# Kernel optimization log

Hardware: AMD Instinct MI355X
Metric: run time of the kernel (lower is better)

## Reference

```python
import jax, jax.numpy as jnp
import numpy as np

B, L, D, V, C = 16384, 50, 128, 91718, 11
H, HD, F = 4, 32, 6
NP = F * (F - 1) // 2  # 15 pairs
CIN = F * D + NP * D   # 2688


def setup_inputs() -> dict:
    key = jax.random.key(0)
    ks = jax.random.split(key, 32)
    inp = {}
    inp['item_id'] = jax.random.randint(ks[0], (B,), 0, V)
    inp['item_mm'] = jax.random.normal(ks[1], (B, D), dtype=jnp.float32)
    inp['likes'] = jax.random.randint(ks[2], (B,), 0, C)
    inp['views'] = jax.random.randint(ks[3], (B,), 0, C)
    inp['item_seq'] = jax.random.randint(ks[4], (B, L), 0, V)
    g = lambda k, shape, s: (jax.random.normal(k, shape, dtype=jnp.float32) * s)
    inp['item_emb'] = g(ks[5], (V, D), 0.02).at[0].set(0.0)  # padding_idx=0
    inp['cate_emb'] = g(ks[6], (C, D), 0.02)
    inp['mm_w'] = g(ks[7], (D, D), (2.0 / D) ** 0.5)
    inp['mm_b'] = jnp.zeros((D,), jnp.float32)
    inp['ln_g'] = jnp.ones((D,), jnp.float32)
    inp['ln_b'] = jnp.zeros((D,), jnp.float32)
    inp['gnn_W'] = g(ks[8], (H, D, HD), (2.0 / (D + HD)) ** 0.5 * 1.414)
    inp['gnn_a'] = g(ks[9], (H, 2 * HD, 1), 0.1)
    inp['se_w1'] = g(ks[10], (F, F // 2), 0.4)
    inp['se_b1'] = jnp.zeros((F // 2,), jnp.float32)
    inp['se_w2'] = g(ks[11], (F // 2, F), 0.4)
    inp['se_b2'] = jnp.zeros((F,), jnp.float32)
    inp['bi_W'] = g(ks[12], (F - 1, D, D), (2.0 / (2 * D)) ** 0.5)
    inp['mlp_w1'] = g(ks[13], (CIN, 512), (2.0 / CIN) ** 0.5)
    inp['mlp_b1'] = jnp.zeros((512,), jnp.float32)
    inp['bn1_g'] = jnp.ones((512,), jnp.float32)
    inp['bn1_b'] = jnp.zeros((512,), jnp.float32)
    inp['mlp_w2'] = g(ks[14], (512, 256), (2.0 / 512) ** 0.5)
    inp['mlp_b2'] = jnp.zeros((256,), jnp.float32)
    inp['bn2_g'] = jnp.ones((256,), jnp.float32)
    inp['bn2_b'] = jnp.zeros((256,), jnp.float32)
    inp['mlp_w3'] = g(ks[15], (256, 1), (2.0 / 256) ** 0.5)
    inp['mlp_b3'] = jnp.zeros((1,), jnp.float32)
    return inp


def _forward(item_id, item_mm, likes, views, item_seq,
             item_emb, cate_emb, mm_w, mm_b, ln_g, ln_b,
             gnn_W, gnn_a, se_w1, se_b1, se_w2, se_b2, bi_W,
             mlp_w1, mlp_b1, bn1_g, bn1_b, mlp_w2, mlp_b2, bn2_g, bn2_b,
             mlp_w3, mlp_b3):
    bsz = item_id.shape[0]
    eps = 1e-5

    user_feat = jnp.zeros((bsz, D), item_mm.dtype)
    like_feat = cate_emb[likes]
    view_feat = cate_emb[views]
    id_feat = item_emb[item_id]

    # mm_proj: Linear -> LayerNorm -> GELU (exact)
    y = item_mm @ mm_w + mm_b
    mu = y.mean(-1, keepdims=True)
    var = y.var(-1, keepdims=True)
    y = (y - mu) * jax.lax.rsqrt(var + eps) * ln_g + ln_b
    img_feat = jax.nn.gelu(y, approximate=False)

    # masked mean pooling of history
    seq_emb = item_emb[item_seq]                          # [B,L,D]
    mask = item_seq == 0
    seq_emb = jnp.where(mask[..., None], 0.0, seq_emb)
    cnt = jnp.clip(jnp.sum((~mask).astype(seq_emb.dtype), axis=1, keepdims=True), 1.0)
    hist_feat = seq_emb.sum(1) / cnt

    x = jnp.stack([user_feat, like_feat, view_feat, id_feat, img_feat, hist_feat], axis=1)  # [B,6,D]

    # GAT over 6-node fully-connected feature graph
    hp = jnp.einsum('bni,hio->bnho', x, gnn_W)            # [B,6,H,HD]
    a1 = gnn_a[:, :HD, 0]                                  # [H,HD]
    a2 = gnn_a[:, HD:, 0]
    ei = jnp.einsum('bnhd,hd->bhn', hp, a1)
    ej = jnp.einsum('bnhd,hd->bhn', hp, a2)
    e = ei[:, :, :, None] + ej[:, :, None, :]             # [B,H,6,6]
    e = jnp.where(e > 0, e, 0.2 * e)                       # LeakyReLU(0.2)
    att = jax.nn.softmax(e, axis=-1)                       # dropout off (eval)
    h_new = jnp.einsum('bhnm,bmho->bnho', att, hp).reshape(bsz, F, D)
    gnn_feat = jax.nn.elu(h_new + x)                       # in_dim == out_dim

    # SENet
    z = gnn_feat.mean(-1)                                  # [B,6]
    w = jax.nn.sigmoid(jax.nn.relu(z @ se_w1 + se_b1) @ se_w2 + se_b2)
    s = gnn_feat * w[..., None]

    # Bilinear ('each'): vid_i = s_i @ W_i, pairs (i,j), j>i
    vid = jnp.einsum('bfd,fde->bfe', s[:, :F - 1], bi_W)   # [B,5,D]
    p = jnp.stack([vid[:, i] * s[:, j] for i in range(F - 1) for j in range(i + 1, F)], axis=1)  # [B,15,D]

    c = jnp.concatenate([gnn_feat.reshape(bsz, -1), p.reshape(bsz, -1)], axis=1)  # [B,2688]

    # MLP with eval-mode BatchNorm (running mean 0, var 1) and dropout off
    bn = lambda t, g_, b_: t * (g_ / jnp.sqrt(1.0 + eps)) + b_
    h1 = jax.nn.gelu(bn(c @ mlp_w1 + mlp_b1, bn1_g, bn1_b), approximate=False)
    h2 = jax.nn.gelu(bn(h1 @ mlp_w2 + mlp_b2, bn2_g, bn2_b), approximate=False)
    out = jax.nn.sigmoid(h2 @ mlp_w3 + mlp_b3)
    return out.squeeze(-1)


def reference(item_id, item_mm, likes, views, item_seq,
              item_emb, cate_emb, mm_w, mm_b, ln_g, ln_b,
              gnn_W, gnn_a, se_w1, se_b1, se_w2, se_b2, bi_W,
              mlp_w1, mlp_b1, bn1_g, bn1_b, mlp_w2, mlp_b2, bn2_g, bn2_b,
              mlp_w3, mlp_b3):
    return _forward(item_id, item_mm, likes, views, item_seq,
                    item_emb, cate_emb, mm_w, mm_b, ln_g, ln_b,
                    gnn_W, gnn_a, se_w1, se_b1, se_w2, se_b2, bi_W,
                    mlp_w1, mlp_b1, bn1_g, bn1_b, mlp_w2, mlp_b2, bn2_g, bn2_b,
                    mlp_w3, mlp_b3)
```

## Files before the change

kernel.cpp:

```cpp
#include <hip/hip_runtime.h>
#include <hip/hip_bf16.h>
#include <cstdint>
#include <cstddef>

#define BB 16384

typedef float  floatx4 __attribute__((ext_vector_type(4)));
typedef __bf16 bf16x8  __attribute__((ext_vector_type(8)));

__device__ __forceinline__ unsigned short f2bf(float f) {
  union { float f; unsigned int u; } v; v.f = f;
  unsigned int r = v.u + 0x7FFFu + ((v.u >> 16) & 1u);
  return (unsigned short)(r >> 16);
}
__device__ __forceinline__ float bf2f(unsigned short h) {
  union { unsigned int u; float f; } v; v.u = ((unsigned int)h) << 16;
  return v.f;
}
__device__ __forceinline__ float gelu_exact(float x) {
  return 0.5f * x * (1.0f + erff(x * 0.7071067811865475f));
}

#define ALOAD16(g, l) \
  __builtin_amdgcn_global_load_lds((const __attribute__((address_space(1))) void*)(g), \
                                   (__attribute__((address_space(3))) void*)(l), 16, 0, 0)

__global__ void k_pack(const float* __restrict__ mm_w, const float* __restrict__ gnn_W,
                       const float* __restrict__ bi_W, const float* __restrict__ item_mm,
                       const float* __restrict__ item_emb,
                       unsigned short* __restrict__ mmwt, unsigned short* __restrict__ wallt,
                       unsigned short* __restrict__ biwt, unsigned short* __restrict__ immb,
                       unsigned short* __restrict__ iembb)
{
  const int total = 2211840 + 2934976;
  for (int id = blockIdx.x * 256 + threadIdx.x; id < total; id += gridDim.x * 256) {
    if (id < 16384) {
      int n = id / 128, k = id % 128;
      mmwt[id] = f2bf(mm_w[k * 128 + n]);
    } else if (id < 32768) {
      int l = id - 16384; int nc = l / 128, k = l % 128;
      wallt[l] = f2bf(gnn_W[(nc >> 5) * 4096 + k * 32 + (nc & 31)]);
    } else if (id < 114688) {
      int l = id - 32768; int f = l / 16384, rr = l % 16384, e = rr / 128, d = rr % 128;
      biwt[l] = f2bf(bi_W[f * 16384 + d * 128 + e]);
    } else if (id < 2211840) {
      int l = id - 114688;
      immb[l] = f2bf(item_mm[l]);
    } else {
      int l = id - 2211840;
      float4 v = ((const float4*)item_emb)[l];
      ushort4 o; o.x = f2bf(v.x); o.y = f2bf(v.y); o.z = f2bf(v.z); o.w = f2bf(v.w);
      ((ushort4*)iembb)[l] = o;
    }
  }
}

__global__ __launch_bounds__(256)
void k_transp2(const float* __restrict__ w1, const float* __restrict__ w2,
               unsigned short* __restrict__ w1t, unsigned short* __restrict__ w2t)
{
  __shared__ float tile[64][65];
  int blk = blockIdx.x;
  const float* in; unsigned short* outp; int R, C, bx, by;
  if (blk < 336) { in = w1; outp = w1t; R = 2688; C = 512; bx = blk % 8; by = blk / 8; }
  else { blk -= 336; in = w2; outp = w2t; R = 512; C = 256; bx = blk % 4; by = blk / 4; }
  const int c0 = bx * 64, r0 = by * 64;
  const int lr = threadIdx.x >> 6;
  const int lc = threadIdx.x & 63;
  #pragma unroll
  for (int i = 0; i < 16; i++) {
    int r = lr + i * 4;
    tile[r][lc] = in[(size_t)(r0 + r) * C + c0 + lc];
  }
  __syncthreads();
  #pragma unroll
  for (int i = 0; i < 16; i++) {
    int c = lr + i * 4;
    outp[(size_t)(c0 + c) * R + r0 + lc] = f2bf(tile[lc][c]);
  }
}

template<int BM, int EPI, bool SWZ>
__global__ __launch_bounds__(512)
void gemm_bt(const unsigned short* __restrict__ A, int lda,
             const unsigned short* __restrict__ Bt, int ldb,
             void* __restrict__ Cp, int ldc, int K,
             const float* __restrict__ bias, const float* __restrict__ bng,
             const float* __restrict__ bnb)
{
  constexpr int WGM = BM / 64;
  constexpr int WGN = 8 / WGM;
  constexpr int TN  = 128 / WGN;
  constexpr int NT  = TN / 16;
  constexpr int NRW = (BM + 128) / 8;
  constexpr int ISS = NRW / 8;

  int bx = blockIdx.x, by = blockIdx.y;
  if constexpr (SWZ) {
    int p = by * gridDim.x + bx;
    int xcd = p & 7, slot = p >> 3;
    bx = slot % gridDim.x;
    by = xcd * (gridDim.y >> 3) + slot / gridDim.x;
  }
  const int n0 = bx * 128;
  const int m0 = by * BM;
  __shared__ __align__(16) unsigned short As[BM * 64];
  __shared__ __align__(16) unsigned short Bs[128 * 64];
  const int t = threadIdx.x;
  const int lane = t & 63, w = t >> 6;
  const int wm = w % WGM, wn = w / WGM;
  const int lr = lane & 15, lq = lane >> 4;

  floatx4 acc[4][NT];
  #pragma unroll
  for (int a = 0; a < 4; a++)
    #pragma unroll
    for (int b = 0; b < NT; b++) acc[a][b] = (floatx4){0.f, 0.f, 0.f, 0.f};

  const int srow = lane >> 3;
  const int schk = (lane & 7) ^ srow;
  const int rb0 = w * NRW;

  for (int k0 = 0; k0 < K; k0 += 64) {
    __syncthreads();
    #pragma unroll
    for (int q = 0; q < ISS; q++) {
      const int rb = rb0 + q * 8;
      if (rb < BM) {
        ALOAD16(A + (size_t)(m0 + rb + srow) * lda + k0 + schk * 8, As + rb * 64);
      } else {
        const int rbb = rb - BM;
        ALOAD16(Bt + (size_t)(n0 + rbb + srow) * ldb + k0 + schk * 8, Bs + rbb * 64);
      }
    }
    __syncthreads();
    #pragma unroll
    for (int ko = 0; ko < 2; ko++) {
      bf16x8 af[4], bfv[NT];
      #pragma unroll
      for (int mt = 0; mt < 4; mt++) {
        const int row = wm * 64 + mt * 16 + lr;
        const int pc = (ko * 4 + lq) ^ (lr & 7);
        af[mt] = __builtin_bit_cast(bf16x8, *(const uint4*)&As[row * 64 + pc * 8]);
      }
      #pragma unroll
      for (int nt = 0; nt < NT; nt++) {
        const int row = wn * TN + nt * 16 + lr;
        const int pc = (ko * 4 + lq) ^ (lr & 7);
        bfv[nt] = __builtin_bit_cast(bf16x8, *(const uint4*)&Bs[row * 64 + pc * 8]);
      }
      #pragma unroll
      for (int mt = 0; mt < 4; mt++)
        #pragma unroll
        for (int nt = 0; nt < NT; nt++)
          acc[mt][nt] = __builtin_amdgcn_mfma_f32_16x16x32_bf16(af[mt], bfv[nt], acc[mt][nt], 0, 0, 0);
    }
  }

  #pragma unroll
  for (int mt = 0; mt < 4; mt++)
    #pragma unroll
    for (int nt = 0; nt < NT; nt++)
      #pragma unroll
      for (int i = 0; i < 4; i++) {
        const int cm = m0 + wm * 64 + mt * 16 + lq * 4 + i;
        const int cn = n0 + wn * TN + nt * 16 + lr;
        float v = acc[mt][nt][i];
        size_t idx = (size_t)cm * ldc + cn;
        float tt = v + bias[cn];
        tt = tt * (bng[cn] * 0.9999950000374997f) + bnb[cn];
        ((unsigned short*)Cp)[idx] = f2bf(gelu_exact(tt));
      }
}

__global__ __launch_bounds__(512)
void k_mmln(const unsigned short* __restrict__ A, const unsigned short* __restrict__ Bt,
            const float* __restrict__ mm_b, const float* __restrict__ ln_g,
            const float* __restrict__ ln_b, unsigned short* __restrict__ xb)
{
  __shared__ __align__(16) char smem[64 * 130 * 4];
  unsigned short* As = (unsigned short*)smem;
  unsigned short* Bs = (unsigned short*)(smem + 8192);
  float* cls = (float*)smem;

  const int t = threadIdx.x, lane = t & 63, w = t >> 6;
  const int lr = lane & 15, lq = lane >> 4;
  const int m0 = blockIdx.x * 64;

  floatx4 acc[4];
  #pragma unroll
  for (int a = 0; a < 4; a++) acc[a] = (floatx4){0.f, 0.f, 0.f, 0.f};

  const int srow = lane >> 3;
  const int schk = (lane & 7) ^ srow;
  const int rb0 = w * 24;

  for (int k0 = 0; k0 < 128; k0 += 64) {
    __syncthreads();
    #pragma unroll
    for (int q = 0; q < 3; q++) {
      const int rb = rb0 + q * 8;
      if (rb < 64) ALOAD16(A + (size_t)(m0 + rb + srow) * 128 + k0 + schk * 8, As + rb * 64);
      else { const int rbb = rb - 64; ALOAD16(Bt + (size_t)(rbb + srow) * 128 + k0 + schk * 8, Bs + rbb * 64); }
    }
    __syncthreads();
    #pragma unroll
    for (int ko = 0; ko < 2; ko++) {
      bf16x8 af[4], bv;
      #pragma unroll
      for (int mt = 0; mt < 4; mt++) {
        const int row = mt * 16 + lr;
        const int pc = (ko * 4 + lq) ^ (lr & 7);
        af[mt] = __builtin_bit_cast(bf16x8, *(const uint4*)&As[row * 64 + pc * 8]);
      }
      {
        const int row = w * 16 + lr;
        const int pc = (ko * 4 + lq) ^ (lr & 7);
        bv = __builtin_bit_cast(bf16x8, *(const uint4*)&Bs[row * 64 + pc * 8]);
      }
      #pragma unroll
      for (int mt = 0; mt < 4; mt++)
        acc[mt] = __builtin_amdgcn_mfma_f32_16x16x32_bf16(af[mt], bv, acc[mt], 0, 0, 0);
    }
  }

  __syncthreads();
  #pragma unroll
  for (int mt = 0; mt < 4; mt++)
    #pragma unroll
    for (int i = 0; i < 4; i++) {
      const int rr = mt * 16 + lq * 4 + i;
      const int cc = w * 16 + lr;
      cls[rr * 130 + cc] = acc[mt][i] + mm_b[cc];
    }
  __syncthreads();

  const float2 g2 = *(const float2*)&ln_g[lane * 2];
  const float2 b2 = *(const float2*)&ln_b[lane * 2];
  #pragma unroll
  for (int rr = 0; rr < 8; rr++) {
    const int r = w * 8 + rr;
    float2 v = *(const float2*)&cls[r * 130 + lane * 2];
    float s = v.x + v.y, s2 = v.x * v.x + v.y * v.y;
    #pragma unroll
    for (int o = 32; o > 0; o >>= 1) { s += __shfl_xor(s, o, 64); s2 += __shfl_xor(s2, o, 64); }
    float mu  = s * (1.0f / 128.0f);
    float var = s2 * (1.0f / 128.0f) - mu * mu;
    float rs  = rsqrtf(var + 1e-5f);
    float t0 = gelu_exact((v.x - mu) * rs * g2.x + b2.x);
    float t1 = gelu_exact((v.y - mu) * rs * g2.y + b2.y);
    unsigned int pk = (unsigned int)f2bf(t0) | ((unsigned int)f2bf(t1) << 16);
    *(unsigned int*)&xb[(size_t)(m0 + r) * 768 + 512 + lane * 2] = pk;
  }
}

__global__ __launch_bounds__(256)
void k_hpatt(const unsigned short* __restrict__ xb, const unsigned short* __restrict__ wallt,
             const float* __restrict__ gnn_a, const float* __restrict__ se_w1,
             const float* __restrict__ se_b1, const float* __restrict__ se_w2,
             const float* __restrict__ se_b2, unsigned short* __restrict__ c,
             unsigned short* __restrict__ sb)
{
  __shared__ __align__(16) char smem[52992];
  unsigned short* As = (unsigned short*)smem;
  unsigned short* Bs = (unsigned short*)(smem + 12288);
  float* hps  = (float*)smem;
  float* eis  = (float*)(smem + 49920);
  float* ejs  = eis + 96;
  float* atts = ejs + 96;

  const int t = threadIdx.x, lane = t & 63, w = t >> 6;
  const int wm = w & 1, wn = w >> 1;
  const int lr = lane & 15, lq = lane >> 4;
  const int m0 = blockIdx.x * 96;

  floatx4 acc[3][4];
  #pragma unroll
  for (int a = 0; a < 3; a++)
    #pragma unroll
    for (int b = 0; b < 4; b++) acc[a][b] = (floatx4){0.f, 0.f, 0.f, 0.f};

  const int srow = lane >> 3;
  const int schk = (lane & 7) ^ srow;
  const int rb0 = w * 56;

  for (int k0 = 0; k0 < 128; k0 += 64) {
    __syncthreads();
    #pragma unroll
    for (int q = 0; q < 7; q++) {
      const int rb = rb0 + q * 8;
      if (rb < 96) ALOAD16(xb + (size_t)(m0 + rb + srow) * 128 + k0 + schk * 8, As + rb * 64);
      else { const int rbb = rb - 96; ALOAD16(wallt + (size_t)(rbb + srow) * 128 + k0 + schk * 8, Bs + rbb * 64); }
    }
    __syncthreads();
    #pragma unroll
    for (int ko = 0; ko < 2; ko++) {
      bf16x8 af[3], bfv[4];
      #pragma unroll
      for (int mt = 0; mt < 3; mt++) {
        const int row = wm * 48 + mt * 16 + lr;
        const int pc = (ko * 4 + lq) ^ (lr & 7);
        af[mt] = __builtin_bit_cast(bf16x8, *(const uint4*)&As[row * 64 + pc * 8]);
      }
      #pragma unroll
      for (int nt = 0; nt < 4; nt++) {
        const int row = wn * 64 + nt * 16 + lr;
        const int pc = (ko * 4 + lq) ^ (lr & 7);
        bfv[nt] = __builtin_bit_cast(bf16x8, *(const uint4*)&Bs[row * 64 + pc * 8]);
      }
      #pragma unroll
      for (int mt = 0; mt < 3; mt++)
        #pragma unroll
        for (int nt = 0; nt < 4; nt++)
          acc[mt][nt] = __builtin_amdgcn_mfma_f32_16x16x32_bf16(af[mt], bfv[nt], acc[mt][nt], 0, 0, 0);
    }
  }

  __syncthreads();
  #pragma unroll
  for (int mt = 0; mt < 3; mt++)
    #pragma unroll
    for (int nt = 0; nt < 4; nt++)
      #pragma unroll
      for (int i = 0; i < 4; i++) {
        const int rr = wm * 48 + mt * 16 + lq * 4 + i;
        const int cc = wn * 64 + nt * 16 + lr;
        hps[rr * 130 + cc] = acc[mt][nt][i];
      }
  __syncthreads();

  for (int it = 0; it < 4; it++) {
    const int lb = w * 4 + it;
    const int b = blockIdx.x * 16 + lb;
    const float* hb = hps + lb * 6 * 130;

    if (lane < 24) {
      int h = lane & 3, n = lane >> 2;
      float e1 = 0.f, e2 = 0.f;
      for (int o = 0; o < 32; o++) {
        float v = hb[n * 130 + h * 32 + o];
        e1 += v * gnn_a[h * 64 + o];
        e2 += v * gnn_a[h * 64 + 32 + o];
      }
      eis[w * 24 + h * 6 + n] = e1; ejs[w * 24 + h * 6 + n] = e2;
    }
    if (lane < 24) {
      int h = lane & 3, i = lane >> 2;
      float ev[6]; float mx = -1e30f;
      #pragma unroll
      for (int j = 0; j < 6; j++) {
        float e = eis[w * 24 + h * 6 + i] + ejs[w * 24 + h * 6 + j];
        e = e > 0.f ? e : 0.2f * e;
        ev[j] = e; mx = fmaxf(mx, e);
      }
      float ssum = 0.f;
      #pragma unroll
      for (int j = 0; j < 6; j++) { ev[j] = expf(ev[j] - mx); ssum += ev[j]; }
      float inv = 1.0f / ssum;
      #pragma unroll
      for (int j = 0; j < 6; j++) atts[w * 144 + h * 36 + i * 6 + j] = ev[j] * inv;
    }

    const int hh = lane >> 4;
    float g0[6], g1[6], zz[6];
    #pragma unroll
    for (int n = 0; n < 6; n++) {
      float hn0 = 0.f, hn1 = 0.f;
      #pragma unroll
      for (int m = 0; m < 6; m++) {
        float a = atts[w * 144 + hh * 36 + n * 6 + m];
        float2 v = *(const float2*)&hb[m * 130 + lane * 2];
        hn0 += a * v.x; hn1 += a * v.y;
      }
      unsigned int xp = *(const unsigned int*)&xb[(size_t)b * 768 + n * 128 + lane * 2];
      float a0 = hn0 + bf2f((unsigned short)(xp & 0xFFFFu));
      float a1 = hn1 + bf2f((unsigned short)(xp >> 16));
      a0 = a0 > 0.f ? a0 : expm1f(a0);
      a1 = a1 > 0.f ? a1 : expm1f(a1);
      g0[n] = a0; g1[n] = a1;
      float zacc = a0 + a1;
      #pragma unroll
      for (int o = 32; o > 0; o >>= 1) zacc += __shfl_xor(zacc, o, 64);
      zz[n] = zacc * (1.0f / 128.0f);
    }

    float rr3[3];
    #pragma unroll
    for (int j = 0; j < 3; j++) {
      float a = se_b1[j];
      #pragma unroll
      for (int n = 0; n < 6; n++) a += zz[n] * se_w1[n * 3 + j];
      rr3[j] = fmaxf(a, 0.f);
    }
    float wse[6];
    #pragma unroll
    for (int n = 0; n < 6; n++) {
      float a = se_b2[n];
      #pragma unroll
      for (int j = 0; j < 3; j++) a += rr3[j] * se_w2[j * 6 + n];
      wse[n] = 1.0f / (1.0f + expf(-a));
    }

    #pragma unroll
    for (int n = 0; n < 6; n++) {
      unsigned int pc = (unsigned int)f2bf(g0[n]) | ((unsigned int)f2bf(g1[n]) << 16);
      unsigned int ps = (unsigned int)f2bf(g0[n] * wse[n]) | ((unsigned int)f2bf(g1[n] * wse[n]) << 16);
      *(unsigned int*)&c[(size_t)b * 2688 + n * 128 + lane * 2]  = pc;
      *(unsigned int*)&sb[(size_t)b * 768 + n * 128 + lane * 2]  = ps;
    }
  }
}

__global__ __launch_bounds__(256)
void gemm_vid(const unsigned short* __restrict__ sbb, const unsigned short* __restrict__ biwt,
              unsigned short* __restrict__ c)
{
  const int z = blockIdx.z;
  const int m0 = blockIdx.y * 128;
  __shared__ __align__(16) unsigned short smem[128 * 130];
  unsigned short* As = smem;
  unsigned short* Bs = smem + 8192;
  const int t = threadIdx.x;
  const int lane = t & 63, w = t >> 6;
  const int wm = w & 1, wn = w >> 1;
  const int lr = lane & 15, lq = lane >> 4;

  floatx4 acc[4][4];
  #pragma unroll
  for (int a = 0; a < 4; a++)
    #pragma unroll
    for (int b = 0; b < 4; b++) acc[a][b] = (floatx4){0.f, 0.f, 0.f, 0.f};

  const int srow = lane >> 3;
  const int schk = (lane & 7) ^ srow;
  const unsigned short* Ag = sbb + (size_t)(m0 + w * 32 + srow) * 768 + z * 128 + schk * 8;
  const unsigned short* Bg = biwt + z * 16384 + (size_t)(w * 32 + srow) * 128 + schk * 8;
  unsigned short* AsW = As + w * 32 * 64;
  unsigned short* BsW = Bs + w * 32 * 64;

  for (int k0 = 0; k0 < 128; k0 += 64) {
    __syncthreads();
    #pragma unroll
    for (int q = 0; q < 4; q++) {
      ALOAD16(Ag + k0 + (size_t)(q * 8) * 768, AsW + q * 512);
      ALOAD16(Bg + k0 + (size_t)(q * 8) * 128, BsW + q * 512);
    }
    __syncthreads();
    #pragma unroll
    for (int ko = 0; ko < 2; ko++) {
      bf16x8 af[4], bfv[4];
      #pragma unroll
      for (int mt = 0; mt < 4; mt++) {
        const int row = wm * 64 + mt * 16 + lr;
        const int pc = (ko * 4 + lq) ^ (lr & 7);
        af[mt] = __builtin_bit_cast(bf16x8, *(const uint4*)&As[row * 64 + pc * 8]);
      }
      #pragma unroll
      for (int nt = 0; nt < 4; nt++) {
        const int row = wn * 64 + nt * 16 + lr;
        const int pc = (ko * 4 + lq) ^ (lr & 7);
        bfv[nt] = __builtin_bit_cast(bf16x8, *(const uint4*)&Bs[row * 64 + pc * 8]);
      }
      #pragma unroll
      for (int mt = 0; mt < 4; mt++)
        #pragma unroll
        for (int nt = 0; nt < 4; nt++)
          acc[mt][nt] = __builtin_amdgcn_mfma_f32_16x16x32_bf16(af[mt], bfv[nt], acc[mt][nt], 0, 0, 0);
    }
  }

  __syncthreads();
  #pragma unroll
  for (int mt = 0; mt < 4; mt++)
    #pragma unroll
    for (int nt = 0; nt < 4; nt++)
      #pragma unroll
      for (int i = 0; i < 4; i++) {
        const int rr = wm * 64 + mt * 16 + lq * 4 + i;
        const int cc = wn * 64 + nt * 16 + lr;
        smem[rr * 130 + cc] = f2bf(acc[mt][nt][i]);
      }
  __syncthreads();

  const int pb0[5] = {0, 5, 9, 12, 14};
  const int npairs = 5 - z;
  const int tot = 128 * 32 * npairs;
  for (int e = t; e < tot; e += 256) {
    const int g  = e & 31;
    const int rp = e >> 5;
    const int p  = rp % npairs;
    const int r  = rp / npairs;
    ushort4 vv = *(const ushort4*)&smem[r * 130 + g * 4];
    ushort4 sv = *(const ushort4*)&sbb[(size_t)(m0 + r) * 768 + (z + 1 + p) * 128 + g * 4];
    ushort4 o;
    o.x = f2bf(bf2f(vv.x) * bf2f(sv.x));
    o.y = f2bf(bf2f(vv.y) * bf2f(sv.y));
    o.z = f2bf(bf2f(vv.z) * bf2f(sv.z));
    o.w = f2bf(bf2f(vv.w) * bf2f(sv.w));
    *(ushort4*)&c[(size_t)(m0 + r) * 2688 + 768 + (size_t)(pb0[z] + p) * 128 + g * 4] = o;
  }
}

__global__ __launch_bounds__(256)
void k_feat(const int* __restrict__ item_id, const int* __restrict__ likes,
            const int* __restrict__ views, const int* __restrict__ item_seq,
            const unsigned short* __restrict__ iembb, const float* __restrict__ cate_emb,
            unsigned short* __restrict__ xb)
{
  const int b = blockIdx.x * 4 + (threadIdx.x >> 6);
  const int lane = threadIdx.x & 63;
  const int half = lane >> 5, ql = lane & 31;
  const size_t base = (size_t)b * 768;
  const int li = likes[b], vi = views[b], id = item_id[b];

  int idxs[25];
  #pragma unroll
  for (int j = 0; j < 25; j++) idxs[j] = item_seq[b * 50 + half + 2 * j];

  float4 hs = make_float4(0.f, 0.f, 0.f, 0.f);
  float cnt = 0.f;
  #pragma unroll
  for (int j = 0; j < 25; j++) {
    const int idx = idxs[j];
    if (idx != 0) {
      cnt += 1.0f;
      ushort4 v = *(const ushort4*)&iembb[(size_t)idx * 128 + ql * 4];
      hs.x += bf2f(v.x); hs.y += bf2f(v.y); hs.z += bf2f(v.z); hs.w += bf2f(v.w);
    }
  }
  cnt  += __shfl_xor(cnt, 32, 64);
  hs.x += __shfl_xor(hs.x, 32, 64);
  hs.y += __shfl_xor(hs.y, 32, 64);
  hs.z += __shfl_xor(hs.z, 32, 64);
  hs.w += __shfl_xor(hs.w, 32, 64);
  const float ic = 1.0f / fmaxf(cnt, 1.0f);

  *(unsigned int*)&xb[base + lane * 2] = 0u;

  {
    const float4 v = *(const float4*)&cate_emb[(size_t)(half ? vi : li) * 128 + ql * 4];
    ushort4 o; o.x = f2bf(v.x); o.y = f2bf(v.y); o.z = f2bf(v.z); o.w = f2bf(v.w);
    *(ushort4*)&xb[base + 128 + half * 128 + ql * 4] = o;
  }
  if (half == 0) {
    *(ushort4*)&xb[base + 384 + ql * 4] =
        *(const ushort4*)&iembb[(size_t)id * 128 + ql * 4];
  } else {
    ushort4 o; o.x = f2bf(hs.x * ic); o.y = f2bf(hs.y * ic);
               o.z = f2bf(hs.z * ic); o.w = f2bf(hs.w * ic);
    *(ushort4*)&xb[base + 640 + ql * 4] = o;
  }
}

__global__ __launch_bounds__(512)
void k_mlp2out(const unsigned short* __restrict__ A, const unsigned short* __restrict__ Bt,
               const float* __restrict__ b2v, const float* __restrict__ bng,
               const float* __restrict__ bnb, const float* __restrict__ w3,
               const float* __restrict__ b3, float* __restrict__ out)
{
  __shared__ __align__(16) char smem[40960];
  unsigned short* As = (unsigned short*)smem;
  unsigned short* Bs = (unsigned short*)(smem + 8192);
  unsigned short* h2s = (unsigned short*)smem;

  const int t = threadIdx.x, lane = t & 63, w = t >> 6;
  const int lr = lane & 15, lq = lane >> 4;
  const int m0 = blockIdx.x * 64;

  floatx4 acc[4][2];
  #pragma unroll
  for (int a = 0; a < 4; a++)
    #pragma unroll
    for (int b = 0; b < 2; b++) acc[a][b] = (floatx4){0.f, 0.f, 0.f, 0.f};

  const int srow = lane >> 3;
  const int schk = (lane & 7) ^ srow;
  const int rb0 = w * 40;

  for (int k0 = 0; k0 < 512; k0 += 64) {
    __syncthreads();
    #pragma unroll
    for (int q = 0; q < 5; q++) {
      const int rb = rb0 + q * 8;
      if (rb < 64) ALOAD16(A + (size_t)(m0 + rb + srow) * 512 + k0 + schk * 8, As + rb * 64);
      else { const int rbb = rb - 64; ALOAD16(Bt + (size_t)(rbb + srow) * 512 + k0 + schk * 8, Bs + rbb * 64); }
    }
    __syncthreads();
    #pragma unroll
    for (int ko = 0; ko < 2; ko++) {
      bf16x8 af[4], bfv[2];
      #pragma unroll
      for (int mt = 0; mt < 4; mt++) {
        const int row = mt * 16 + lr;
        const int pc = (ko * 4 + lq) ^ (lr & 7);
        af[mt] = __builtin_bit_cast(bf16x8, *(const uint4*)&As[row * 64 + pc * 8]);
      }
      #pragma unroll
      for (int nt = 0; nt < 2; nt++) {
        const int row = w * 32 + nt * 16 + lr;
        const int pc = (ko * 4 + lq) ^ (lr & 7);
        bfv[nt] = __builtin_bit_cast(bf16x8, *(const uint4*)&Bs[row * 64 + pc * 8]);
      }
      #pragma unroll
      for (int mt = 0; mt < 4; mt++)
        #pragma unroll
        for (int nt = 0; nt < 2; nt++)
          acc[mt][nt] = __builtin_amdgcn_mfma_f32_16x16x32_bf16(af[mt], bfv[nt], acc[mt][nt], 0, 0, 0);
    }
  }

  __syncthreads();
  #pragma unroll
  for (int mt = 0; mt < 4; mt++)
    #pragma unroll
    for (int nt = 0; nt < 2; nt++)
      #pragma unroll
      for (int i = 0; i < 4; i++) {
        const int rr = mt * 16 + lq * 4 + i;
        const int cc = w * 32 + nt * 16 + lr;
        float tt = acc[mt][nt][i] + b2v[cc];
        tt = tt * (bng[cc] * 0.9999950000374997f) + bnb[cc];
        h2s[rr * 264 + cc] = f2bf(gelu_exact(tt));
      }
  __syncthreads();

  const float4 w4 = *(const float4*)&w3[lane * 4];
  #pragma unroll
  for (int rr = 0; rr < 8; rr++) {
    const int r = w * 8 + rr;
    ushort4 v = *(const ushort4*)&h2s[r * 264 + lane * 4];
    float a = bf2f(v.x) * w4.x + bf2f(v.y) * w4.y + bf2f(v.z) * w4.z + bf2f(v.w) * w4.w;
    #pragma unroll
    for (int o = 32; o > 0; o >>= 1) a += __shfl_xor(a, o, 64);
    if (lane == 0) out[m0 + r] = 1.0f / (1.0f + expf(-(a + b3[0])));
  }
}

#define OFF_MMWT   0ull
#define OFF_WALLT  32768ull
#define OFF_BIWT   65536ull
#define OFF_W1T    229376ull
#define OFF_W2T    2981888ull
#define OFF_IMMB   3244032ull
#define OFF_XB     7438336ull
#define OFF_SB     57769984ull
#define OFF_C      82935808ull
#define OFF_IEMB   179404800ull

extern "C" void kernel_launch(void* const* d_in, const int* in_sizes, int n_in,
                              void* d_out, int out_size, void* d_ws, size_t ws_size,
                              hipStream_t stream)
{
  const int*   item_id  = (const int*)  d_in[0];
  const float* item_mm  = (const float*)d_in[1];
  const int*   likes    = (const int*)  d_in[2];
  const int*   views    = (const int*)  d_in[3];
  const int*   item_seq = (const int*)  d_in[4];
  const float* item_emb = (const float*)d_in[5];
  const float* cate_emb = (const float*)d_in[6];
  const float* mm_w     = (const float*)d_in[7];
  const float* mm_b     = (const float*)d_in[8];
  const float* ln_g     = (const float*)d_in[9];
  const float* ln_b     = (const float*)d_in[10];
  const float* gnn_W    = (const float*)d_in[11];
  const float* gnn_a    = (const float*)d_in[12];
  const float* se_w1    = (const float*)d_in[13];
  const float* se_b1    = (const float*)d_in[14];
  const float* se_w2    = (const float*)d_in[15];
  const float* se_b2    = (const float*)d_in[16];
  const float* bi_W     = (const float*)d_in[17];
  const float* mlp_w1   = (const float*)d_in[18];
  const float* mlp_b1   = (const float*)d_in[19];
  const float* bn1_g    = (const float*)d_in[20];
  const float* bn1_b    = (const float*)d_in[21];
  const float* mlp_w2   = (const float*)d_in[22];
  const float* mlp_b2   = (const float*)d_in[23];
  const float* bn2_g    = (const float*)d_in[24];
  const float* bn2_b    = (const float*)d_in[25];
  const float* mlp_w3   = (const float*)d_in[26];
  const float* mlp_b3   = (const float*)d_in[27];
  float* out = (float*)d_out;

  char* ws = (char*)d_ws;
  unsigned short* mmwt  = (unsigned short*)(ws + OFF_MMWT);
  unsigned short* wallt = (unsigned short*)(ws + OFF_WALLT);
  unsigned short* biwt  = (unsigned short*)(ws + OFF_BIWT);
  unsigned short* w1t   = (unsigned short*)(ws + OFF_W1T);
  unsigned short* w2t   = (unsigned short*)(ws + OFF_W2T);
  unsigned short* immb  = (unsigned short*)(ws + OFF_IMMB);
  unsigned short* xb    = (unsigned short*)(ws + OFF_XB);
  unsigned short* sbb   = (unsigned short*)(ws + OFF_SB);
  unsigned short* cbuf  = (unsigned short*)(ws + OFF_C);
  unsigned short* h1b   = (unsigned short*)(ws + OFF_XB);
  unsigned short* iembb = (unsigned short*)(ws + OFF_IEMB);

  k_pack<<<4096, 256, 0, stream>>>(mm_w, gnn_W, bi_W, item_mm, item_emb,
                                   mmwt, wallt, biwt, immb, iembb);
  k_transp2<<<368, 256, 0, stream>>>(mlp_w1, mlp_w2, w1t, w2t);
  k_feat<<<BB / 4, 256, 0, stream>>>(item_id, likes, views, item_seq, iembb, cate_emb, xb);
  k_mmln<<<256, 512, 0, stream>>>(immb, mmwt, mm_b, ln_g, ln_b, xb);
  k_hpatt<<<1024, 256, 0, stream>>>(xb, wallt, gnn_a, se_w1, se_b1, se_w2, se_b2, cbuf, sbb);
  gemm_vid<<<dim3(1, 128, 5), 256, 0, stream>>>(sbb, biwt, cbuf);
  gemm_bt<128, 3, true><<<dim3(4, 128), 512, 0, stream>>>(cbuf, 2688, w1t, 2688,
      h1b, 512, 2688, mlp_b1, bn1_g, bn1_b);
  k_mlp2out<<<256, 512, 0, stream>>>(h1b, w2t, mlp_b2, bn2_g, bn2_b, mlp_w3, mlp_b3, out);
}
```

Measured before the change: 347.2 us.

## Deepen MLP1 GEMM K-tile to 128 and move small weight transposes into tiled kernel

The MLP1 GEMM is specialised to fixed sizes and loads a K depth of 128 per iteration instead of 64. This halves the number of barrier-separated load/compute rounds, at the cost of doubling LDS use to 64 KB per block, which may reduce occupancy. The bi_W and mm_w transposes move from the strided element-wise pack loop into the shared-memory tiled transpose kernel. The item_mm bf16 conversion is also vectorised to float4 loads.

```diff
diff --git a/kernel.cpp b/kernel.cpp
--- a/kernel.cpp
+++ b/kernel.cpp
@@ -25,29 +25,23 @@
   __builtin_amdgcn_global_load_lds((const __attribute__((address_space(1))) void*)(g), \
                                    (__attribute__((address_space(3))) void*)(l), 16, 0, 0)
 
-__global__ void k_pack(const float* __restrict__ mm_w, const float* __restrict__ gnn_W,
-                       const float* __restrict__ bi_W, const float* __restrict__ item_mm,
+__global__ void k_pack(const float* __restrict__ gnn_W, const float* __restrict__ item_mm,
                        const float* __restrict__ item_emb,
-                       unsigned short* __restrict__ mmwt, unsigned short* __restrict__ wallt,
-                       unsigned short* __restrict__ biwt, unsigned short* __restrict__ immb,
+                       unsigned short* __restrict__ wallt, unsigned short* __restrict__ immb,
                        unsigned short* __restrict__ iembb)
 {
-  const int total = 2211840 + 2934976;
+  const int total = 16384 + 524288 + 2934976;
   for (int id = blockIdx.x * 256 + threadIdx.x; id < total; id += gridDim.x * 256) {
     if (id < 16384) {
-      int n = id / 128, k = id % 128;
-      mmwt[id] = f2bf(mm_w[k * 128 + n]);
-    } else if (id < 32768) {
-      int l = id - 16384; int nc = l / 128, k = l % 128;
-      wallt[l] = f2bf(gnn_W[(nc >> 5) * 4096 + k * 32 + (nc & 31)]);
-    } else if (id < 114688) {
-      int l = id - 32768; int f = l / 16384, rr = l % 16384, e = rr / 128, d = rr % 128;
-      biwt[l] = f2bf(bi_W[f * 16384 + d * 128 + e]);
-    } else if (id < 2211840) {
-      int l = id - 114688;
-      immb[l] = f2bf(item_mm[l]);
+      int nc = id / 128, k = id % 128;
+      wallt[id] = f2bf(gnn_W[(nc >> 5) * 4096 + k * 32 + (nc & 31)]);
+    } else if (id < 540672) {
+      int l = id - 16384;
+      float4 v = ((const float4*)item_mm)[l];
+      ushort4 o; o.x = f2bf(v.x); o.y = f2bf(v.y); o.z = f2bf(v.z); o.w = f2bf(v.w);
+      ((ushort4*)immb)[l] = o;
     } else {
-      int l = id - 2211840;
+      int l = id - 540672;
       float4 v = ((const float4*)item_emb)[l];
       ushort4 o; o.x = f2bf(v.x); o.y = f2bf(v.y); o.z = f2bf(v.z); o.w = f2bf(v.w);
       ((ushort4*)iembb)[l] = o;
@@ -57,13 +51,20 @@
 
 __global__ __launch_bounds__(256)
 void k_transp2(const float* __restrict__ w1, const float* __restrict__ w2,
-               unsigned short* __restrict__ w1t, unsigned short* __restrict__ w2t)
+               const float* __restrict__ bi_W, const float* __restrict__ mm_w,
+               unsigned short* __restrict__ w1t, unsigned short* __restrict__ w2t,
+               unsigned short* __restrict__ biwt, unsigned short* __restrict__ mmwt)
 {
   __shared__ float tile[64][65];
   int blk = blockIdx.x;
   const float* in; unsigned short* outp; int R, C, bx, by;
-  if (blk < 336) { in = w1; outp = w1t; R = 2688; C = 512; bx = blk % 8; by = blk / 8; }
-  else { blk -= 336; in = w2; outp = w2t; R = 512; C = 256; bx = blk % 4; by = blk / 4; }
+  if (blk < 336)      { in = w1; outp = w1t; R = 2688; C = 512; bx = blk % 8; by = blk / 8; }
+  else if (blk < 368) { blk -= 336; in = w2; outp = w2t; R = 512; C = 256; bx = blk % 4; by = blk / 4; }
+  else if (blk < 388) { blk -= 368; int f = blk / 4; int r2 = blk % 4;
+                        in = bi_W + f * 16384; outp = biwt + f * 16384;
+                        R = 128; C = 128; bx = r2 % 2; by = r2 / 2; }
+  else                { blk -= 388; in = mm_w; outp = mmwt; R = 128; C = 128;
+                        bx = blk % 2; by = blk / 2; }
   const int c0 = bx * 64, r0 = by * 64;
   const int lr = threadIdx.x >> 6;
   const int lc = threadIdx.x & 63;
@@ -80,79 +81,67 @@
   }
 }
 
-template<int BM, int EPI, bool SWZ>
 __global__ __launch_bounds__(512)
-void gemm_bt(const unsigned short* __restrict__ A, int lda,
-             const unsigned short* __restrict__ Bt, int ldb,
-             void* __restrict__ Cp, int ldc, int K,
-             const float* __restrict__ bias, const float* __restrict__ bng,
-             const float* __restrict__ bnb)
-{
-  constexpr int WGM = BM / 64;
-  constexpr int WGN = 8 / WGM;
-  constexpr int TN  = 128 / WGN;
-  constexpr int NT  = TN / 16;
-  constexpr int NRW = (BM + 128) / 8;
-  constexpr int ISS = NRW / 8;
-
-  int bx = blockIdx.x, by = blockIdx.y;
-  if constexpr (SWZ) {
-    int p = by * gridDim.x + bx;
-    int xcd = p & 7, slot = p >> 3;
-    bx = slot % gridDim.x;
-    by = xcd * (gridDim.y >> 3) + slot / gridDim.x;
-  }
+void gemm_mlp1(const unsigned short* __restrict__ A, const unsigned short* __restrict__ Bt,
+               unsigned short* __restrict__ Cp,
+               const float* __restrict__ bias, const float* __restrict__ bng,
+               const float* __restrict__ bnb)
+{
+  int p = blockIdx.y * gridDim.x + blockIdx.x;
+  int xcd = p & 7, slot = p >> 3;
+  const int bx = slot % gridDim.x;
+  const int by = xcd * (gridDim.y >> 3) + slot / gridDim.x;
   const int n0 = bx * 128;
-  const int m0 = by * BM;
-  __shared__ __align__(16) unsigned short As[BM * 64];
-  __shared__ __align__(16) unsigned short Bs[128 * 64];
-  const int t = threadIdx.x;
-  const int lane = t & 63, w = t >> 6;
-  const int wm = w % WGM, wn = w / WGM;
+  const int m0 = by * 128;
+
+  __shared__ __align__(16) unsigned short As[128 * 128];
+  __shared__ __align__(16) unsigned short Bs[128 * 128];
+  const int t = threadIdx.x, lane = t & 63, w = t >> 6;
+  const int wm = w & 1, wn = w >> 1;
   const int lr = lane & 15, lq = lane >> 4;
 
-  floatx4 acc[4][NT];
+  floatx4 acc[4][2];
   #pragma unroll
   for (int a = 0; a < 4; a++)
     #pragma unroll
-    for (int b = 0; b < NT; b++) acc[a][b] = (floatx4){0.f, 0.f, 0.f, 0.f};
-
-  const int srow = lane >> 3;
-  const int schk = (lane & 7) ^ srow;
-  const int rb0 = w * NRW;
-
-  for (int k0 = 0; k0 < K; k0 += 64) {
-    __syncthreads();
-    #pragma unroll
-    for (int q = 0; q < ISS; q++) {
-      const int rb = rb0 + q * 8;
-      if (rb < BM) {
-        ALOAD16(A + (size_t)(m0 + rb + srow) * lda + k0 + schk * 8, As + rb * 64);
+    for (int b = 0; b < 2; b++) acc[a][b] = (floatx4){0.f, 0.f, 0.f, 0.f};
+
+  const int srow = lane >> 4;
+  const int rb0 = w * 32;
+
+  for (int k0 = 0; k0 < 2688; k0 += 128) {
+    __syncthreads();
+    #pragma unroll
+    for (int q = 0; q < 8; q++) {
+      const int rb = rb0 + q * 4;
+      const int row = rb + srow;
+      const int schk = (lane & 15) ^ (row & 7);
+      if (rb < 128) {
+        ALOAD16(A + (size_t)(m0 + row) * 2688 + k0 + schk * 8, As + rb * 128);
       } else {
-        const int rbb = rb - BM;
-        ALOAD16(Bt + (size_t)(n0 + rbb + srow) * ldb + k0 + schk * 8, Bs + rbb * 64);
-      }
-    }
-    __syncthreads();
-    #pragma unroll
-    for (int ko = 0; ko < 2; ko++) {
-      bf16x8 af[4], bfv[NT];
+        ALOAD16(Bt + (size_t)(n0 + row - 128) * 2688 + k0 + schk * 8, Bs + (rb - 128) * 128);
+      }
+    }
+    __syncthreads();
+    #pragma unroll
+    for (int ko = 0; ko < 4; ko++) {
+      bf16x8 af[4], bfv[2];
       #pragma unroll
       for (int mt = 0; mt < 4; mt++) {
         const int row = wm * 64 + mt * 16 + lr;
-        const int pc = (ko * 4 + lq) ^ (lr & 7);
-        af[mt] = __builtin_bit_cast(bf16x8, *(const uint4*)&As[row * 64 + pc * 8]);
-      }
-      #pragma unroll
-      for (int nt = 0; nt < NT; nt++) {
-        const int row = wn * TN + nt * 16 + lr;
-        const int pc = (ko * 4 + lq) ^ (lr & 7);
-        bfv[nt] = __builtin_bit_cast(bf16x8, *(const uint4*)&Bs[row * 64 + pc * 8]);
+        const int pc = (ko * 4 + lq) ^ (row & 7);
+        af[mt] = __builtin_bit_cast(bf16x8, *(const uint4*)&As[row * 128 + pc * 8]);
+      }
+      #pragma unroll
+      for (int nt = 0; nt < 2; nt++) {
+        const int row = wn * 32 + nt * 16 + lr;
+        const int pc = (ko * 4 + lq) ^ (row & 7);
+        bfv[nt] = __builtin_bit_cast(bf16x8, *(const uint4*)&Bs[row * 128 + pc * 8]);
       }
       #pragma unroll
       for (int mt = 0; mt < 4; mt++)
         #pragma unroll
-        for (int nt = 0; nt < NT; nt++)
+        for (int nt = 0; nt < 2; nt++)
           acc[mt][nt] = __builtin_amdgcn_mfma_f32_16x16x32_bf16(af[mt], bfv[nt], acc[mt][nt], 0, 0, 0);
     }
   }
@@ -160,16 +149,14 @@
   #pragma unroll
   for (int mt = 0; mt < 4; mt++)
     #pragma unroll
-    for (int nt = 0; nt < NT; nt++)
+    for (int nt = 0; nt < 2; nt++)
       #pragma unroll
       for (int i = 0; i < 4; i++) {
         const int cm = m0 + wm * 64 + mt * 16 + lq * 4 + i;
-        const int cn = n0 + wn * TN + nt * 16 + lr;
-        float v = acc[mt][nt][i];
-        size_t idx = (size_t)cm * ldc + cn;
-        float tt = v + bias[cn];
+        const int cn = n0 + wn * 32 + nt * 16 + lr;
+        float tt = acc[mt][nt][i] + bias[cn];
         tt = tt * (bng[cn] * 0.9999950000374997f) + bnb[cn];
-        ((unsigned short*)Cp)[idx] = f2bf(gelu_exact(tt));
+        Cp[(size_t)cm * 512 + cn] = f2bf(gelu_exact(tt));
       }
 }
 
@@ -694,14 +681,12 @@
   unsigned short* h1b   = (unsigned short*)(ws + OFF_XB);
   unsigned short* iembb = (unsigned short*)(ws + OFF_IEMB);
 
-  k_pack<<<4096, 256, 0, stream>>>(mm_w, gnn_W, bi_W, item_mm, item_emb,
-                                   mmwt, wallt, biwt, immb, iembb);
-  k_transp2<<<368, 256, 0, stream>>>(mlp_w1, mlp_w2, w1t, w2t);
+  k_pack<<<4096, 256, 0, stream>>>(gnn_W, item_mm, item_emb, wallt, immb, iembb);
+  k_transp2<<<392, 256, 0, stream>>>(mlp_w1, mlp_w2, bi_W, mm_w, w1t, w2t, biwt, mmwt);
   k_feat<<<BB / 4, 256, 0, stream>>>(item_id, likes, views, item_seq, iembb, cate_emb, xb);
   k_mmln<<<256, 512, 0, stream>>>(immb, mmwt, mm_b, ln_g, ln_b, xb);
   k_hpatt<<<1024, 256, 0, stream>>>(xb, wallt, gnn_a, se_w1, se_b1, se_w2, se_b2, cbuf, sbb);
   gemm_vid<<<dim3(1, 128, 5), 256, 0, stream>>>(sbb, biwt, cbuf);
-  gemm_bt<128, 3, true><<<dim3(4, 128), 512, 0, stream>>>(cbuf, 2688, w1t, 2688,
-      h1b, 512, 2688, mlp_b1, bn1_g, bn1_b);
+  gemm_mlp1<<<dim3(4, 128), 512, 0, stream>>>(cbuf, w1t, h1b, mlp_b1, bn1_g, bn1_b);
   k_mlp2out<<<256, 512, 0, stream>>>(h1b, w2t, mlp_b2, bn2_g, bn2_b, mlp_w3, mlp_b3, out);
 }
```

Result: no change. 350.6 us (+1.0%).
